# Optimization experiments

Hardware: AMD Instinct MI355X
Metric: run time of the kernel (lower is better)

Reference implementation:

```python
import jax, jax.numpy as jnp
import numpy as np

B, TX, TY, D, H, DK, DFF, L, V = 64, 200, 100, 512, 8, 64, 2048, 4, 30


def _ln(x, g, b, eps=1e-5):
    m = x.mean(-1, keepdims=True)
    v = x.var(-1, keepdims=True)  # biased, matches torch LayerNorm
    return (x - m) * jax.lax.rsqrt(v + eps) * g + b


def _mha(k_in, v_in, q_in, qkv, pw, pb, pad_mask, causal):
    # qkv: [3, H, DK, D] (torch Linear layout [out, in]); scale uses C = d_model
    scale = float(q_in.shape[-1]) ** 0.5
    Q = jnp.einsum('btd,hkd->bhtk', q_in, qkv[0])
    K = jnp.einsum('bsd,hkd->bhsk', k_in, qkv[1])
    Vv = jnp.einsum('bsd,hvd->bhsv', v_in, qkv[2])
    W = jnp.einsum('bhtk,bhsk->bhts', Q, K) / scale  # [B,H,T,S]
    if causal:
        tril = jnp.tril(jnp.ones((q_in.shape[1], k_in.shape[1]), bool))
        W = jnp.where(tril, W, -jnp.inf)
    if pad_mask is not None:
        W = jnp.where(pad_mask[:, None] == 1, -jnp.inf, W)
    A = jax.nn.softmax(W, axis=-1)
    out = jnp.einsum('bhts,bhsv->bhtv', A, Vv)
    b_, h_, t_, dv = out.shape
    out = out.transpose(0, 2, 1, 3).reshape(b_, t_, h_ * dv)  # concat heads
    return out @ pw.T + pb


def _attn_block(k, v, q, qkv, pw, pb, g, b, pad_mask, causal):
    kn, vn, qn = _ln(k, g, b), _ln(v, g, b), _ln(q, g, b)
    # NOTE: residual from the NORMED query, as in the original code
    return qn + _mha(kn, vn, qn, qkv, pw, pb, pad_mask, causal)


def _ff_block(x, w1, b1, w2, b2, g, b):
    h = jax.nn.relu(_ln(x, g, b) @ w1.T + b1)
    return x + h @ w2.T + b2


def _forward(x, y, enc_qkv, enc_proj_w, enc_proj_b, enc_ln1_g, enc_ln1_b,
             enc_ff_w1, enc_ff_b1, enc_ff_w2, enc_ff_b2, enc_ln2_g, enc_ln2_b,
             dec_sa_qkv, dec_sa_proj_w, dec_sa_proj_b, dec_ln1_g, dec_ln1_b,
             dec_ca_qkv, dec_ca_proj_w, dec_ca_proj_b, dec_ln2_g, dec_ln2_b,
             dec_ff_w1, dec_ff_b1, dec_ff_w2, dec_ff_b2, dec_ln3_g, dec_ln3_b,
             ll_w, ll_b, x_mask, y_mask):
    enc = x
    for i in range(L):
        enc = _attn_block(enc, enc, enc, enc_qkv[i], enc_proj_w[i], enc_proj_b[i],
                          enc_ln1_g[i], enc_ln1_b[i], x_mask, False)
        enc = _ff_block(enc, enc_ff_w1[i], enc_ff_b1[i], enc_ff_w2[i], enc_ff_b2[i],
                        enc_ln2_g[i], enc_ln2_b[i])
    dec = y
    for i in range(L):
        dec = _attn_block(dec, dec, dec, dec_sa_qkv[i], dec_sa_proj_w[i], dec_sa_proj_b[i],
                          dec_ln1_g[i], dec_ln1_b[i], y_mask, True)
        dec = _attn_block(enc, enc, dec, dec_ca_qkv[i], dec_ca_proj_w[i], dec_ca_proj_b[i],
                          dec_ln2_g[i], dec_ln2_b[i], None, False)
        dec = _ff_block(dec, dec_ff_w1[i], dec_ff_b1[i], dec_ff_w2[i], dec_ff_b2[i],
                        dec_ln3_g[i], dec_ln3_b[i])
    return dec @ ll_w.T + ll_b


def setup_inputs() -> dict:
    key = jax.random.key(0)
    ks = iter(jax.random.split(key, 64))

    def nrm(shape, s=0.02):
        return jax.random.normal(next(ks), shape, jnp.float32) * s

    return dict(
        x=nrm((B, TX, D), 1.0), y=nrm((B, TY, D), 1.0),
        x_mask=jnp.zeros((B, TX, TX), jnp.int32),
        y_mask=jnp.zeros((B, TY, TY), jnp.int32),
        enc_qkv=nrm((L, 3, H, DK, D)), enc_proj_w=nrm((L, D, D)), enc_proj_b=jnp.zeros((L, D)),
        enc_ln1_g=jnp.ones((L, D)), enc_ln1_b=jnp.zeros((L, D)),
        enc_ff_w1=nrm((L, DFF, D)), enc_ff_b1=jnp.zeros((L, DFF)),
        enc_ff_w2=nrm((L, D, DFF)), enc_ff_b2=jnp.zeros((L, D)),
        enc_ln2_g=jnp.ones((L, D)), enc_ln2_b=jnp.zeros((L, D)),
        dec_sa_qkv=nrm((L, 3, H, DK, D)), dec_sa_proj_w=nrm((L, D, D)), dec_sa_proj_b=jnp.zeros((L, D)),
        dec_ln1_g=jnp.ones((L, D)), dec_ln1_b=jnp.zeros((L, D)),
        dec_ca_qkv=nrm((L, 3, H, DK, D)), dec_ca_proj_w=nrm((L, D, D)), dec_ca_proj_b=jnp.zeros((L, D)),
        dec_ln2_g=jnp.ones((L, D)), dec_ln2_b=jnp.zeros((L, D)),
        dec_ff_w1=nrm((L, DFF, D)), dec_ff_b1=jnp.zeros((L, DFF)),
        dec_ff_w2=nrm((L, D, DFF)), dec_ff_b2=jnp.zeros((L, D)),
        dec_ln3_g=jnp.ones((L, D)), dec_ln3_b=jnp.zeros((L, D)),
        ll_w=nrm((V, D)), ll_b=jnp.zeros((V,)),
    )


def reference(x, y, x_mask, y_mask, enc_qkv, enc_proj_w, enc_proj_b, enc_ln1_g, enc_ln1_b,
              enc_ff_w1, enc_ff_b1, enc_ff_w2, enc_ff_b2, enc_ln2_g, enc_ln2_b,
              dec_sa_qkv, dec_sa_proj_w, dec_sa_proj_b, dec_ln1_g, dec_ln1_b,
              dec_ca_qkv, dec_ca_proj_w, dec_ca_proj_b, dec_ln2_g, dec_ln2_b,
              dec_ff_w1, dec_ff_b1, dec_ff_w2, dec_ff_b2, dec_ln3_g, dec_ln3_b,
              ll_w, ll_b):
    return _forward(x, y, enc_qkv, enc_proj_w, enc_proj_b, enc_ln1_g, enc_ln1_b,
                    enc_ff_w1, enc_ff_b1, enc_ff_w2, enc_ff_b2, enc_ln2_g, enc_ln2_b,
                    dec_sa_qkv, dec_sa_proj_w, dec_sa_proj_b, dec_ln1_g, dec_ln1_b,
                    dec_ca_qkv, dec_ca_proj_w, dec_ca_proj_b, dec_ln2_g, dec_ln2_b,
                    dec_ff_w1, dec_ff_b1, dec_ff_w2, dec_ff_b2, dec_ln3_g, dec_ln3_b,
                    ll_w, ll_b, x_mask, y_mask)
```

## Files before the change

### kernel.cpp

```cpp
#include <hip/hip_runtime.h>
#include <math.h>

#define B_SZ   64
#define TX_SZ  200
#define TY_SZ  100
#define D_MODEL 512
#define H_SZ   8
#define DK_SZ  64
#define DFF_SZ 2048
#define L_SZ   4
#define V_SZ   30

#define NEG_BIG -1.0e30f

#define KSTR  68
#define VSTR  212
#define PSTR  204
#define KOFF  0
#define VOFF  (200 * KSTR)
#define POFF  (VOFF + 64 * VSTR)
#define SMEMU (POFF + 4 * 16 * PSTR)

typedef unsigned short u16;
typedef __attribute__((ext_vector_type(8))) short short8;
typedef __attribute__((ext_vector_type(4))) short short4t;
typedef __attribute__((ext_vector_type(4))) float f32x4;
typedef __attribute__((ext_vector_type(4))) unsigned short u16x4;

__device__ __forceinline__ float b2f(u16 h) {
    union { unsigned int u; float f; } v; v.u = ((unsigned int)h) << 16; return v.f;
}
__device__ __forceinline__ u16 f2b(float f) {
    union { float f; unsigned int u; } v; v.f = f;
    unsigned int r = v.u + 0x7fffu + ((v.u >> 16) & 1u);
    return (u16)(r >> 16);
}
__device__ __forceinline__ short8 ld8(const u16* p) {
    short4t a = *(const short4t*)p;
    short4t b = *(const short4t*)(p + 4);
    return __builtin_shufflevector(a, b, 0, 1, 2, 3, 4, 5, 6, 7);
}

#define GLD16(gp, lp) __builtin_amdgcn_global_load_lds( \
    (const __attribute__((address_space(1))) unsigned int*)(gp), \
    (__attribute__((address_space(3))) unsigned int*)(lp), 16, 0, 0)

__global__ __launch_bounds__(256)
void castw_kernel(const float* __restrict__ in, u16* __restrict__ out, int n4) {
    int i = blockIdx.x * 256 + threadIdx.x;
    if (i < n4) {
        f32x4 v = ((const f32x4*)in)[i];
        u16x4 o;
        o.x = f2b(v.x); o.y = f2b(v.y); o.z = f2b(v.z); o.w = f2b(v.w);
        ((u16x4*)out)[i] = o;
    }
}

__global__ __launch_bounds__(256)
void ln_kernel(const float* __restrict__ in, const float* __restrict__ g,
               const float* __restrict__ b, float* outf, u16* outb, int rows) {
    int row = blockIdx.x * 4 + (threadIdx.x >> 6);
    int lane = threadIdx.x & 63;
    if (row >= rows) return;
    const f32x4* xr = (const f32x4*)(in + (size_t)row * D_MODEL);
    f32x4 v0 = xr[lane];
    f32x4 v1 = xr[lane + 64];
    float s  = v0.x + v0.y + v0.z + v0.w + v1.x + v1.y + v1.z + v1.w;
    float ss = v0.x*v0.x + v0.y*v0.y + v0.z*v0.z + v0.w*v0.w
             + v1.x*v1.x + v1.y*v1.y + v1.z*v1.z + v1.w*v1.w;
    #pragma unroll
    for (int off = 1; off < 64; off <<= 1) {
        s  += __shfl_xor(s, off, 64);
        ss += __shfl_xor(ss, off, 64);
    }
    float mean = s * (1.0f / D_MODEL);
    float var  = ss * (1.0f / D_MODEL) - mean * mean;
    float rstd = rsqrtf(var + 1e-5f);
    f32x4 g0 = ((const f32x4*)g)[lane],      g1 = ((const f32x4*)g)[lane + 64];
    f32x4 b0 = ((const f32x4*)b)[lane],      b1 = ((const f32x4*)b)[lane + 64];
    f32x4 o0, o1;
    o0.x = (v0.x - mean) * rstd * g0.x + b0.x;
    o0.y = (v0.y - mean) * rstd * g0.y + b0.y;
    o0.z = (v0.z - mean) * rstd * g0.z + b0.z;
    o0.w = (v0.w - mean) * rstd * g0.w + b0.w;
    o1.x = (v1.x - mean) * rstd * g1.x + b1.x;
    o1.y = (v1.y - mean) * rstd * g1.y + b1.y;
    o1.z = (v1.z - mean) * rstd * g1.z + b1.z;
    o1.w = (v1.w - mean) * rstd * g1.w + b1.w;
    if (outf) {
        f32x4* of = (f32x4*)(outf + (size_t)row * D_MODEL);
        of[lane] = o0; of[lane + 64] = o1;
    }
    if (outb) {
        u16x4* ob = (u16x4*)(outb + (size_t)row * D_MODEL);
        u16x4 p0, p1;
        p0.x = f2b(o0.x); p0.y = f2b(o0.y); p0.z = f2b(o0.z); p0.w = f2b(o0.w);
        p1.x = f2b(o1.x); p1.y = f2b(o1.y); p1.z = f2b(o1.z); p1.w = f2b(o1.w);
        ob[lane] = p0; ob[lane + 64] = p1;
    }
}

template<int BN>
__global__ __launch_bounds__(256)
void gemm_mfma_t(const u16* __restrict__ A, int lda,
                 const u16* __restrict__ W, int ldw,
                 float* outf, int ldcf, u16* outb, int ldcb,
                 const float* __restrict__ bias,
                 const float* __restrict__ resid, int ldr,
                 int relu, int K) {
    constexpr int NJ = BN / 32;
    __shared__ u16 Alds[128 * 32];
    __shared__ u16 Blds[BN * 32];
    const int tid  = threadIdx.x;
    const int wave = tid >> 6, lane = tid & 63;
    const int lr = lane & 15, lq = lane >> 4;
    const int wm = (wave >> 1) * 64, wn = (wave & 1) * (BN / 2);
    const int m0 = blockIdx.y * 128, n0 = blockIdx.x * BN;
    const int grow = tid >> 2;
    const int gcol = (tid & 3) * 8;
    const int woff = wave * 512;

    f32x4 zero = {0.f, 0.f, 0.f, 0.f};
    f32x4 acc[4][NJ];
    #pragma unroll
    for (int i = 0; i < 4; ++i)
        #pragma unroll
        for (int j = 0; j < NJ; ++j) acc[i][j] = zero;

    const u16* Ag = A + (size_t)m0 * lda;
    const u16* Wg = W + (size_t)n0 * ldw;

    for (int k0 = 0; k0 < K; k0 += 32) {
        GLD16(Ag + (size_t)grow * lda + k0 + gcol,        &Alds[woff]);
        GLD16(Ag + (size_t)(64 + grow) * lda + k0 + gcol, &Alds[2048 + woff]);
        GLD16(Wg + (size_t)grow * ldw + k0 + gcol,        &Blds[woff]);
        if (BN == 128)
            GLD16(Wg + (size_t)(64 + grow) * ldw + k0 + gcol, &Blds[2048 + woff]);
        __syncthreads();
        short8 af[4], bfr[NJ];
        #pragma unroll
        for (int i = 0; i < 4; ++i)
            af[i] = *(const short8*)&Alds[(wm + i * 16 + lr) * 32 + lq * 8];
        #pragma unroll
        for (int j = 0; j < NJ; ++j)
            bfr[j] = *(const short8*)&Blds[(wn + j * 16 + lr) * 32 + lq * 8];
        #pragma unroll
        for (int i = 0; i < 4; ++i)
            #pragma unroll
            for (int j = 0; j < NJ; ++j)
                acc[i][j] = __builtin_amdgcn_mfma_f32_16x16x32_bf16(af[i], bfr[j], acc[i][j], 0, 0, 0);
        __syncthreads();
    }

    #pragma unroll
    for (int i = 0; i < 4; ++i) {
        #pragma unroll
        for (int r = 0; r < 4; ++r) {
            int m = m0 + wm + i * 16 + lq * 4 + r;
            #pragma unroll
            for (int j = 0; j < NJ; ++j) {
                int n = n0 + wn + j * 16 + lr;
                float c = acc[i][j][r];
                if (bias)  c += bias[n];
                if (resid) c += resid[(size_t)m * ldr + n];
                if (relu)  c = fmaxf(c, 0.f);
                if (outf) outf[(size_t)m * ldcf + n] = c;
                if (outb) outb[(size_t)m * ldcb + n] = f2b(c);
            }
        }
    }
}

__global__ __launch_bounds__(256)
void attn_kernel(u16* __restrict__ Q, int ldq, const u16* __restrict__ K, int ldk,
                 const u16* __restrict__ V, int ldv,
                 const int* __restrict__ mask, int T, int S, int causal, float rscale) {
    __shared__ u16 smem[SMEMU];
    u16* Kl = smem + KOFF;
    u16* Vt = smem + VOFF;
    u16* Pl = smem + POFF;

    const int bh = blockIdx.x;
    const int h = bh % H_SZ, b = bh / H_SZ;
    const int tid = threadIdx.x, wave = tid >> 6, lane = tid & 63;
    const int lm = lane & 15, quad = lane >> 4;

    const u16* Kg = K + (size_t)(b * S) * ldk + h * DK_SZ;
    const u16* Vg = V + (size_t)(b * S) * ldv + h * DK_SZ;
    u16* Qg = Q + (size_t)(b * T) * ldq + h * DK_SZ;

    const int stiles = (S + 15) >> 4;
    const int Scols = stiles << 4;
    const int Pcap = (Scols < PSTR) ? Scols : PSTR;

    for (int i4 = tid * 4; i4 < S * DK_SZ; i4 += 1024) {
        int s = i4 >> 6, d = i4 & 63;
        u16x4 kv = *(const u16x4*)(Kg + (size_t)s * ldk + d);
        *(u16x4*)(Kl + s * KSTR + d) = kv;
        u16x4 vv = *(const u16x4*)(Vg + (size_t)s * ldv + d);
        Vt[(d + 0) * VSTR + s] = vv.x;
        Vt[(d + 1) * VSTR + s] = vv.y;
        Vt[(d + 2) * VSTR + s] = vv.z;
        Vt[(d + 3) * VSTR + s] = vv.w;
    }
    int pad = Scols - S;
    for (int i = tid; i < pad * DK_SZ; i += 256) {
        int d = i / pad, s = S + (i % pad);
        Vt[d * VSTR + s] = 0;
    }
    __syncthreads();

    const short8 zero8 = {0, 0, 0, 0, 0, 0, 0, 0};
    const f32x4 zerof = {0.f, 0.f, 0.f, 0.f};
    u16* Pw = Pl + wave * (16 * PSTR);

    for (int t0 = wave * 16; t0 < T; t0 += 64) {
        int qr = t0 + lm; if (qr >= T) qr = T - 1;
        const u16* qrow = Qg + (size_t)qr * ldq;
        short8 qa0 = *(const short8*)(qrow + quad * 8);
        short8 qa1 = *(const short8*)(qrow + 32 + quad * 8);

        f32x4 sc[13];
        #pragma unroll
        for (int st = 0; st < 13; ++st) if (st < stiles) {
            int srow = st * 16 + lm; if (srow >= S) srow = S - 1;
            const u16* kp = Kl + srow * KSTR + quad * 8;
            short8 kb0 = ld8(kp);
            short8 kb1 = ld8(kp + 32);
            f32x4 c = zerof;
            c = __builtin_amdgcn_mfma_f32_16x16x32_bf16(qa0, kb0, c, 0, 0, 0);
            c = __builtin_amdgcn_mfma_f32_16x16x32_bf16(qa1, kb1, c, 0, 0, 0);
            sc[st] = c;
        }

        float mx[4] = {NEG_BIG, NEG_BIG, NEG_BIG, NEG_BIG};
        #pragma unroll
        for (int st = 0; st < 13; ++st) if (st < stiles) {
            int s = st * 16 + lm;
            int smi = (s < S) ? s : S - 1;
            #pragma unroll
            for (int r = 0; r < 4; ++r) {
                int t = t0 + quad * 4 + r;
                int tc = (t < T) ? t : T - 1;
                bool valid = (s < S) && (!causal || s <= t);
                if (valid && mask) valid = (mask[(size_t)(b * T + tc) * S + smi] != 1);
                float f = valid ? sc[st][r] * rscale : NEG_BIG;
                sc[st][r] = f;
                mx[r] = fmaxf(mx[r], f);
            }
        }
        #pragma unroll
        for (int r = 0; r < 4; ++r) {
            #pragma unroll
            for (int off = 1; off < 16; off <<= 1)
                mx[r] = fmaxf(mx[r], __shfl_xor(mx[r], off, 64));
        }

        float sum[4] = {0.f, 0.f, 0.f, 0.f};
        #pragma unroll
        for (int st = 0; st < 13; ++st) if (st < stiles) {
            int col = st * 16 + lm;
            #pragma unroll
            for (int r = 0; r < 4; ++r) {
                float p = __expf(sc[st][r] - mx[r]);
                sum[r] += p;
                if (col < PSTR) Pw[(quad * 4 + r) * PSTR + col] = f2b(p);
            }
        }
        float rden[4];
        #pragma unroll
        for (int r = 0; r < 4; ++r) {
            #pragma unroll
            for (int off = 1; off < 16; off <<= 1)
                sum[r] += __shfl_xor(sum[r], off, 64);
            rden[r] = (sum[r] > 0.f) ? 1.0f / sum[r] : 0.f;
        }

        f32x4 ov[4] = {zerof, zerof, zerof, zerof};
        for (int k0 = 0; k0 < Pcap; k0 += 32) {
            int nq = (Pcap - k0) >> 3;
            short8 pa = (quad < nq) ? ld8(Pw + lm * PSTR + k0 + quad * 8) : zero8;
            #pragma unroll
            for (int dt = 0; dt < 4; ++dt) {
                short8 vb = (quad < nq)
                    ? ld8(Vt + (dt * 16 + lm) * VSTR + k0 + quad * 8)
                    : zero8;
                ov[dt] = __builtin_amdgcn_mfma_f32_16x16x32_bf16(pa, vb, ov[dt], 0, 0, 0);
            }
        }

        #pragma unroll
        for (int r = 0; r < 4; ++r) {
            int t = t0 + quad * 4 + r;
            if (t < T) {
                u16* orow = Qg + (size_t)t * ldq;
                #pragma unroll
                for (int dt = 0; dt < 4; ++dt)
                    orow[dt * 16 + lm] = f2b(ov[dt][r] * rden[r]);
            }
        }
    }
}

__global__ __launch_bounds__(256)
void logits_kernel(const float* __restrict__ X, const float* __restrict__ Wl,
                   const float* __restrict__ bl, float* __restrict__ out, int rows) {
    int idx = blockIdx.x * 256 + threadIdx.x;
    if (idx >= rows * V_SZ) return;
    int row = idx / V_SZ, v = idx % V_SZ;
    const f32x4* xr = (const f32x4*)(X + (size_t)row * D_MODEL);
    const f32x4* wr = (const f32x4*)(Wl + (size_t)v * D_MODEL);
    float acc = bl[v];
    #pragma unroll 4
    for (int k = 0; k < D_MODEL / 4; ++k) {
        f32x4 a = xr[k], w = wr[k];
        acc += a.x * w.x + a.y * w.y + a.z * w.z + a.w * w.w;
    }
    out[idx] = acc;
}

extern "C" void kernel_launch(void* const* d_in, const int* in_sizes, int n_in,
                              void* d_out, int out_size, void* d_ws, size_t ws_size,
                              hipStream_t stream) {
    const float* x          = (const float*)d_in[0];
    const float* y          = (const float*)d_in[1];
    const int*   x_mask     = (const int*)d_in[2];
    const int*   y_mask     = (const int*)d_in[3];
    const float* enc_qkv    = (const float*)d_in[4];
    const float* enc_proj_w = (const float*)d_in[5];
    const float* enc_proj_b = (const float*)d_in[6];
    const float* enc_ln1_g  = (const float*)d_in[7];
    const float* enc_ln1_b  = (const float*)d_in[8];
    const float* enc_ff_w1  = (const float*)d_in[9];
    const float* enc_ff_b1  = (const float*)d_in[10];
    const float* enc_ff_w2  = (const float*)d_in[11];
    const float* enc_ff_b2  = (const float*)d_in[12];
    const float* enc_ln2_g  = (const float*)d_in[13];
    const float* enc_ln2_b  = (const float*)d_in[14];
    const float* dec_sa_qkv    = (const float*)d_in[15];
    const float* dec_sa_proj_w = (const float*)d_in[16];
    const float* dec_sa_proj_b = (const float*)d_in[17];
    const float* dec_ln1_g  = (const float*)d_in[18];
    const float* dec_ln1_b  = (const float*)d_in[19];
    const float* dec_ca_qkv    = (const float*)d_in[20];
    const float* dec_ca_proj_w = (const float*)d_in[21];
    const float* dec_ca_proj_b = (const float*)d_in[22];
    const float* dec_ln2_g  = (const float*)d_in[23];
    const float* dec_ln2_b  = (const float*)d_in[24];
    const float* dec_ff_w1  = (const float*)d_in[25];
    const float* dec_ff_b1  = (const float*)d_in[26];
    const float* dec_ff_w2  = (const float*)d_in[27];
    const float* dec_ff_b2  = (const float*)d_in[28];
    const float* dec_ln3_g  = (const float*)d_in[29];
    const float* dec_ln3_b  = (const float*)d_in[30];
    const float* ll_w       = (const float*)d_in[31];
    const float* ll_b       = (const float*)d_in[32];

    const int ME = B_SZ * TX_SZ;
    const int MD = B_SZ * TY_SZ;
    const float rscale = 1.0f / sqrtf((float)D_MODEL);

    char* base = (char*)d_ws;
    size_t off = 0;
    auto alloc = [&](size_t bytes) {
        void* p = base + off;
        off = (off + bytes + 63) & ~(size_t)63;
        return p;
    };
    float* A_enc = (float*)alloc((size_t)ME * D_MODEL * 4);
    float* A_dec = (float*)alloc((size_t)MD * D_MODEL * 4);
    float* N1f   = (float*)alloc((size_t)ME * D_MODEL * 4);
    u16*   N1b   = (u16*)  alloc((size_t)ME * D_MODEL * 2);
    u16*   NQb   = (u16*)  alloc((size_t)MD * D_MODEL * 2);
    u16*   BIG   = (u16*)  alloc((size_t)ME * DFF_SZ * 2);
    u16*   Wa    = (u16*)  alloc((size_t)DFF_SZ * D_MODEL * 2);
    u16*   Wb2   = (u16*)  alloc((size_t)DFF_SZ * D_MODEL * 2);
    u16* QKVb = BIG;
    u16* Hb   = BIG;
    u16* KVb  = BIG;
    u16* Qca  = BIG + (size_t)ME * 1024;

    auto castw = [&](const float* in, u16* out, int n) {
        int n4 = n / 4;
        hipLaunchKernelGGL(castw_kernel, dim3((n4 + 255) / 256), dim3(256), 0, stream, in, out, n4);
    };
    auto ln = [&](const float* in, const float* g, const float* b,
                  float* outf, u16* outb, int rows) {
        hipLaunchKernelGGL(ln_kernel, dim3(rows / 4), dim3(256), 0, stream, in, g, b, outf, outb, rows);
    };
    auto gemm = [&](const u16* A, int lda, const u16* W, int ldw, int M, int N, int K,
                    float* outf, int ldcf, u16* outb, int ldcb,
                    const float* bias, const float* resid, int ldr, int relu) {
        int blocks128 = (M / 128) * (N / 128);
        if (blocks128 < 256) {
            dim3 grid(N / 64, M / 128);
            hipLaunchKernelGGL((gemm_mfma_t<64>), grid, dim3(256), 0, stream,
                               A, lda, W, ldw, outf, ldcf, outb, ldcb, bias, resid, ldr, relu, K);
        } else {
            dim3 grid(N / 128, M / 128);
            hipLaunchKernelGGL((gemm_mfma_t<128>), grid, dim3(256), 0, stream,
                               A, lda, W, ldw, outf, ldcf, outb, ldcb, bias, resid, ldr, relu, K);
        }
    };
    auto attn = [&](u16* Q, int ldq, const u16* K, int ldk, const u16* V, int ldv,
                    const int* mask, int T, int S, int causal) {
        hipLaunchKernelGGL(attn_kernel, dim3(B_SZ * H_SZ), dim3(256), 0, stream,
                           Q, ldq, K, ldk, V, ldv, mask, T, S, causal, rscale);
    };

    const int WQKV = 3 * D_MODEL * D_MODEL;
    const int WDD  = D_MODEL * D_MODEL;
    const int WFF  = DFF_SZ * D_MODEL;

    for (int l = 0; l < L_SZ; ++l) {
        const float* src = (l == 0) ? x : A_enc;
        castw(enc_qkv + (size_t)l * WQKV, Wa, WQKV);
        ln(src, enc_ln1_g + l * D_MODEL, enc_ln1_b + l * D_MODEL, N1f, N1b, ME);
        gemm(N1b, 512, Wa, 512, ME, 1536, 512, nullptr, 0, QKVb, 1536, nullptr, nullptr, 0, 0);
        attn(QKVb, 1536, QKVb + 512, 1536, QKVb + 1024, 1536, x_mask, TX_SZ, TX_SZ, 0);
        castw(enc_proj_w + (size_t)l * WDD, Wa, WDD);
        gemm(QKVb, 1536, Wa, 512, ME, 512, 512, A_enc, 512, nullptr, 0,
             enc_proj_b + l * D_MODEL, N1f, 512, 0);
        ln(A_enc, enc_ln2_g + l * D_MODEL, enc_ln2_b + l * D_MODEL, nullptr, N1b, ME);
        castw(enc_ff_w1 + (size_t)l * WFF, Wa, WFF);
        gemm(N1b, 512, Wa, 512, ME, 2048, 512, nullptr, 0, Hb, 2048,
             enc_ff_b1 + l * DFF_SZ, nullptr, 0, 1);
        castw(enc_ff_w2 + (size_t)l * WFF, Wb2, WFF);
        gemm(Hb, 2048, Wb2, 2048, ME, 512, 2048, A_enc, 512, nullptr, 0,
             enc_ff_b2 + l * D_MODEL, A_enc, 512, 0);
    }

    for (int l = 0; l < L_SZ; ++l) {
        const float* src = (l == 0) ? y : A_dec;
        castw(dec_sa_qkv + (size_t)l * WQKV, Wa, WQKV);
        ln(src, dec_ln1_g + l * D_MODEL, dec_ln1_b + l * D_MODEL, N1f, N1b, MD);
        gemm(N1b, 512, Wa, 512, MD, 1536, 512, nullptr, 0, QKVb, 1536, nullptr, nullptr, 0, 0);
        attn(QKVb, 1536, QKVb + 512, 1536, QKVb + 1024, 1536, y_mask, TY_SZ, TY_SZ, 1);
        castw(dec_sa_proj_w + (size_t)l * WDD, Wa, WDD);
        gemm(QKVb, 1536, Wa, 512, MD, 512, 512, A_dec, 512, nullptr, 0,
             dec_sa_proj_b + l * D_MODEL, N1f, 512, 0);
        ln(A_enc, dec_ln2_g + l * D_MODEL, dec_ln2_b + l * D_MODEL, nullptr, N1b, ME);
        ln(A_dec, dec_ln2_g + l * D_MODEL, dec_ln2_b + l * D_MODEL, N1f, NQb, MD);
        castw(dec_ca_qkv + (size_t)l * WQKV, Wa, WDD);
        gemm(NQb, 512, Wa, 512, MD, 512, 512, nullptr, 0, Qca, 512, nullptr, nullptr, 0, 0);
        castw(dec_ca_qkv + (size_t)l * WQKV + WDD, Wa, 2 * WDD);
        gemm(N1b, 512, Wa, 512, ME, 1024, 512, nullptr, 0, KVb, 1024, nullptr, nullptr, 0, 0);
        attn(Qca, 512, KVb, 1024, KVb + 512, 1024, nullptr, TY_SZ, TX_SZ, 0);
        castw(dec_ca_proj_w + (size_t)l * WDD, Wa, WDD);
        gemm(Qca, 512, Wa, 512, MD, 512, 512, A_dec, 512, nullptr, 0,
             dec_ca_proj_b + l * D_MODEL, N1f, 512, 0);
        ln(A_dec, dec_ln3_g + l * D_MODEL, dec_ln3_b + l * D_MODEL, nullptr, N1b, MD);
        castw(dec_ff_w1 + (size_t)l * WFF, Wa, WFF);
        gemm(N1b, 512, Wa, 512, MD, 2048, 512, nullptr, 0, Hb, 2048,
             dec_ff_b1 + l * DFF_SZ, nullptr, 0, 1);
        castw(dec_ff_w2 + (size_t)l * WFF, Wb2, WFF);
        gemm(Hb, 2048, Wb2, 2048, MD, 512, 2048, A_dec, 512, nullptr, 0,
             dec_ff_b2 + l * D_MODEL, A_dec, 512, 0);
    }

    {
        int total = MD * V_SZ;
        hipLaunchKernelGGL(logits_kernel, dim3((total + 255) / 256), dim3(256), 0, stream,
                           A_dec, ll_w, ll_b, (float*)d_out, MD);
    }
    (void)in_sizes; (void)n_in; (void)out_size; (void)ws_size;
}
```

Baseline: 3.197 ms.

## Write V transposed from QKV GEMM epilogue and split attention over query tiles

The QKV and KV GEMM epilogues now scatter the V columns directly into a per-(batch,head) transposed buffer, so attention no longer stages and transposes K/V in LDS. The attention grid is split into 64-row query tiles per (batch,head), with K and Vt read straight from global memory, and causal tiles skip key tiles past the diagonal. This removes the per-block LDS transpose and raises parallelism. The cost is scattered strided stores in the GEMM epilogue, uncached global K/V reads repeated across tiles, and an extra pad kernel for the decoder case.

New measurement: 3.468 ms. 8.5% more time.

```diff
diff --git a/kernel.cpp b/kernel.cpp
--- a/kernel.cpp
+++ b/kernel.cpp
@@ -13,13 +13,8 @@
 
 #define NEG_BIG -1.0e30f
 
-#define KSTR  68
-#define VSTR  212
 #define PSTR  204
-#define KOFF  0
-#define VOFF  (200 * KSTR)
-#define POFF  (VOFF + 64 * VSTR)
-#define SMEMU (POFF + 4 * 16 * PSTR)
+#define ATT_LDSU (4 * 16 * PSTR)
 
 typedef unsigned short u16;
 typedef __attribute__((ext_vector_type(8))) short short8;
@@ -53,6 +48,16 @@
         u16x4 o;
         o.x = f2b(v.x); o.y = f2b(v.y); o.z = f2b(v.z); o.w = f2b(v.w);
         ((u16x4*)out)[i] = o;
+    }
+}
+
+__global__ __launch_bounds__(256)
+void vtpad_kernel(u16* __restrict__ Vt, int spad, int S, int nrows) {
+    int pad = spad - S;
+    int i = blockIdx.x * 256 + threadIdx.x;
+    if (i < nrows * pad) {
+        int r = i / pad, c = i - r * pad;
+        Vt[(size_t)r * spad + S + c] = 0;
     }
 }
 
@@ -107,7 +112,9 @@
                  float* outf, int ldcf, u16* outb, int ldcb,
                  const float* __restrict__ bias,
                  const float* __restrict__ resid, int ldr,
-                 int relu, int K) {
+                 int relu, int K,
+                 u16* __restrict__ vtout, int vt_n0, int vt_T,
+                 unsigned rT, int vt_spad) {
     constexpr int NJ = BN / 32;
     __shared__ u16 Alds[128 * 32];
     __shared__ u16 Blds[BN * 32];
@@ -165,7 +172,14 @@
                 if (resid) c += resid[(size_t)m * ldr + n];
                 if (relu)  c = fmaxf(c, 0.f);
                 if (outf) outf[(size_t)m * ldcf + n] = c;
-                if (outb) outb[(size_t)m * ldcb + n] = f2b(c);
+                if (vtout && n >= vt_n0) {
+                    int hd = n - vt_n0;
+                    int bq = (int)(((unsigned)m * rT) >> 22);
+                    int sq = m - bq * vt_T;
+                    vtout[((size_t)((bq << 3) + (hd >> 6)) * 64 + (hd & 63)) * vt_spad + sq] = f2b(c);
+                } else if (outb) {
+                    outb[(size_t)m * ldcb + n] = f2b(c);
+                }
             }
         }
     }
@@ -173,131 +187,113 @@
 
 __global__ __launch_bounds__(256)
 void attn_kernel(u16* __restrict__ Q, int ldq, const u16* __restrict__ K, int ldk,
-                 const u16* __restrict__ V, int ldv,
+                 const u16* __restrict__ Vt, int spad,
                  const int* __restrict__ mask, int T, int S, int causal, float rscale) {
-    __shared__ u16 smem[SMEMU];
-    u16* Kl = smem + KOFF;
-    u16* Vt = smem + VOFF;
-    u16* Pl = smem + POFF;
-
-    const int bh = blockIdx.x;
-    const int h = bh % H_SZ, b = bh / H_SZ;
+    __shared__ u16 Pl[ATT_LDSU];
+    const int tile = blockIdx.x, bh = blockIdx.y;
+    const int h = bh & 7, b = bh >> 3;
     const int tid = threadIdx.x, wave = tid >> 6, lane = tid & 63;
     const int lm = lane & 15, quad = lane >> 4;
+    const int t0 = tile * 64 + wave * 16;
+    if (t0 >= T) return;
 
     const u16* Kg = K + (size_t)(b * S) * ldk + h * DK_SZ;
-    const u16* Vg = V + (size_t)(b * S) * ldv + h * DK_SZ;
+    const u16* Vg = Vt + (size_t)bh * 64 * spad;
     u16* Qg = Q + (size_t)(b * T) * ldq + h * DK_SZ;
 
     const int stiles = (S + 15) >> 4;
-    const int Scols = stiles << 4;
-    const int Pcap = (Scols < PSTR) ? Scols : PSTR;
-
-    for (int i4 = tid * 4; i4 < S * DK_SZ; i4 += 1024) {
-        int s = i4 >> 6, d = i4 & 63;
-        u16x4 kv = *(const u16x4*)(Kg + (size_t)s * ldk + d);
-        *(u16x4*)(Kl + s * KSTR + d) = kv;
-        u16x4 vv = *(const u16x4*)(Vg + (size_t)s * ldv + d);
-        Vt[(d + 0) * VSTR + s] = vv.x;
-        Vt[(d + 1) * VSTR + s] = vv.y;
-        Vt[(d + 2) * VSTR + s] = vv.z;
-        Vt[(d + 3) * VSTR + s] = vv.w;
-    }
-    int pad = Scols - S;
-    for (int i = tid; i < pad * DK_SZ; i += 256) {
-        int d = i / pad, s = S + (i % pad);
-        Vt[d * VSTR + s] = 0;
-    }
-    __syncthreads();
+    int stmax = stiles;
+    if (causal) { int c = (t0 >> 4) + 1; if (c < stmax) stmax = c; }
+    const int Scap8 = (S + 7) & ~7;
+    int Pcap = stmax * 16; if (Pcap > Scap8) Pcap = Scap8;
+
+    u16* Pw = Pl + wave * (16 * PSTR);
+
+    int qr = t0 + lm; if (qr >= T) qr = T - 1;
+    const u16* qrow = Qg + (size_t)qr * ldq;
+    short8 qa0 = *(const short8*)(qrow + quad * 8);
+    short8 qa1 = *(const short8*)(qrow + 32 + quad * 8);
 
     const short8 zero8 = {0, 0, 0, 0, 0, 0, 0, 0};
     const f32x4 zerof = {0.f, 0.f, 0.f, 0.f};
-    u16* Pw = Pl + wave * (16 * PSTR);
-
-    for (int t0 = wave * 16; t0 < T; t0 += 64) {
-        int qr = t0 + lm; if (qr >= T) qr = T - 1;
-        const u16* qrow = Qg + (size_t)qr * ldq;
-        short8 qa0 = *(const short8*)(qrow + quad * 8);
-        short8 qa1 = *(const short8*)(qrow + 32 + quad * 8);
-
-        f32x4 sc[13];
-        #pragma unroll
-        for (int st = 0; st < 13; ++st) if (st < stiles) {
-            int srow = st * 16 + lm; if (srow >= S) srow = S - 1;
-            const u16* kp = Kl + srow * KSTR + quad * 8;
-            short8 kb0 = ld8(kp);
-            short8 kb1 = ld8(kp + 32);
-            f32x4 c = zerof;
-            c = __builtin_amdgcn_mfma_f32_16x16x32_bf16(qa0, kb0, c, 0, 0, 0);
-            c = __builtin_amdgcn_mfma_f32_16x16x32_bf16(qa1, kb1, c, 0, 0, 0);
-            sc[st] = c;
-        }
-
-        float mx[4] = {NEG_BIG, NEG_BIG, NEG_BIG, NEG_BIG};
-        #pragma unroll
-        for (int st = 0; st < 13; ++st) if (st < stiles) {
-            int s = st * 16 + lm;
-            int smi = (s < S) ? s : S - 1;
-            #pragma unroll
-            for (int r = 0; r < 4; ++r) {
-                int t = t0 + quad * 4 + r;
-                int tc = (t < T) ? t : T - 1;
-                bool valid = (s < S) && (!causal || s <= t);
-                if (valid && mask) valid = (mask[(size_t)(b * T + tc) * S + smi] != 1);
-                float f = valid ? sc[st][r] * rscale : NEG_BIG;
-                sc[st][r] = f;
-                mx[r] = fmaxf(mx[r], f);
-            }
-        }
-        #pragma unroll
-        for (int r = 0; r < 4; ++r) {
-            #pragma unroll
-            for (int off = 1; off < 16; off <<= 1)
-                mx[r] = fmaxf(mx[r], __shfl_xor(mx[r], off, 64));
-        }
-
-        float sum[4] = {0.f, 0.f, 0.f, 0.f};
-        #pragma unroll
-        for (int st = 0; st < 13; ++st) if (st < stiles) {
-            int col = st * 16 + lm;
-            #pragma unroll
-            for (int r = 0; r < 4; ++r) {
-                float p = __expf(sc[st][r] - mx[r]);
-                sum[r] += p;
-                if (col < PSTR) Pw[(quad * 4 + r) * PSTR + col] = f2b(p);
-            }
-        }
-        float rden[4];
-        #pragma unroll
-        for (int r = 0; r < 4; ++r) {
-            #pragma unroll
-            for (int off = 1; off < 16; off <<= 1)
-                sum[r] += __shfl_xor(sum[r], off, 64);
-            rden[r] = (sum[r] > 0.f) ? 1.0f / sum[r] : 0.f;
-        }
-
-        f32x4 ov[4] = {zerof, zerof, zerof, zerof};
-        for (int k0 = 0; k0 < Pcap; k0 += 32) {
-            int nq = (Pcap - k0) >> 3;
-            short8 pa = (quad < nq) ? ld8(Pw + lm * PSTR + k0 + quad * 8) : zero8;
-            #pragma unroll
-            for (int dt = 0; dt < 4; ++dt) {
-                short8 vb = (quad < nq)
-                    ? ld8(Vt + (dt * 16 + lm) * VSTR + k0 + quad * 8)
-                    : zero8;
-                ov[dt] = __builtin_amdgcn_mfma_f32_16x16x32_bf16(pa, vb, ov[dt], 0, 0, 0);
-            }
-        }
-
+
+    f32x4 sc[13];
+    #pragma unroll
+    for (int st = 0; st < 13; ++st) if (st < stmax) {
+        int srow = st * 16 + lm; if (srow >= S) srow = S - 1;
+        const u16* kp = Kg + (size_t)srow * ldk + quad * 8;
+        short8 kb0 = *(const short8*)kp;
+        short8 kb1 = *(const short8*)(kp + 32);
+        f32x4 c = zerof;
+        c = __builtin_amdgcn_mfma_f32_16x16x32_bf16(qa0, kb0, c, 0, 0, 0);
+        c = __builtin_amdgcn_mfma_f32_16x16x32_bf16(qa1, kb1, c, 0, 0, 0);
+        sc[st] = c;
+    }
+
+    float mx[4] = {NEG_BIG, NEG_BIG, NEG_BIG, NEG_BIG};
+    #pragma unroll
+    for (int st = 0; st < 13; ++st) if (st < stmax) {
+        int s = st * 16 + lm;
+        int smi = (s < S) ? s : S - 1;
         #pragma unroll
         for (int r = 0; r < 4; ++r) {
             int t = t0 + quad * 4 + r;
-            if (t < T) {
-                u16* orow = Qg + (size_t)t * ldq;
-                #pragma unroll
-                for (int dt = 0; dt < 4; ++dt)
-                    orow[dt * 16 + lm] = f2b(ov[dt][r] * rden[r]);
-            }
+            int tc = (t < T) ? t : T - 1;
+            bool valid = (s < S) && (!causal || s <= t);
+            if (valid && mask) valid = (mask[(size_t)(b * T + tc) * S + smi] != 1);
+            float f = valid ? sc[st][r] * rscale : NEG_BIG;
+            sc[st][r] = f;
+            mx[r] = fmaxf(mx[r], f);
+        }
+    }
+    #pragma unroll
+    for (int r = 0; r < 4; ++r) {
+        #pragma unroll
+        for (int off = 1; off < 16; off <<= 1)
+            mx[r] = fmaxf(mx[r], __shfl_xor(mx[r], off, 64));
+    }
+
+    float sum[4] = {0.f, 0.f, 0.f, 0.f};
+    #pragma unroll
+    for (int st = 0; st < 13; ++st) if (st < stmax) {
+        int col = st * 16 + lm;
+        #pragma unroll
+        for (int r = 0; r < 4; ++r) {
+            float p = __expf(sc[st][r] - mx[r]);
+            sum[r] += p;
+            if (col < PSTR) Pw[(quad * 4 + r) * PSTR + col] = f2b(p);
+        }
+    }
+    float rden[4];
+    #pragma unroll
+    for (int r = 0; r < 4; ++r) {
+        #pragma unroll
+        for (int off = 1; off < 16; off <<= 1)
+            sum[r] += __shfl_xor(sum[r], off, 64);
+        rden[r] = (sum[r] > 0.f) ? 1.0f / sum[r] : 0.f;
+    }
+
+    f32x4 ov[4] = {zerof, zerof, zerof, zerof};
+    for (int k0 = 0; k0 < Pcap; k0 += 32) {
+        int nq = (Pcap - k0) >> 3;
+        short8 pa = (quad < nq) ? ld8(Pw + lm * PSTR + k0 + quad * 8) : zero8;
+        #pragma unroll
+        for (int dt = 0; dt < 4; ++dt) {
+            short8 vb = (quad < nq)
+                ? *(const short8*)(Vg + (size_t)(dt * 16 + lm) * spad + k0 + quad * 8)
+                : zero8;
+            ov[dt] = __builtin_amdgcn_mfma_f32_16x16x32_bf16(pa, vb, ov[dt], 0, 0, 0);
+        }
+    }
+
+    #pragma unroll
+    for (int r = 0; r < 4; ++r) {
+        int t = t0 + quad * 4 + r;
+        if (t < T) {
+            u16* orow = Qg + (size_t)t * ldq;
+            #pragma unroll
+            for (int dt = 0; dt < 4; ++dt)
+                orow[dt * 16 + lm] = f2b(ov[dt][r] * rden[r]);
         }
     }
 }
@@ -359,6 +355,8 @@
     const int ME = B_SZ * TX_SZ;
     const int MD = B_SZ * TY_SZ;
     const float rscale = 1.0f / sqrtf((float)D_MODEL);
+    const unsigned rT200 = (1u << 22) / 200 + 1;
+    const unsigned rT100 = (1u << 22) / 100 + 1;
 
     char* base = (char*)d_ws;
     size_t off = 0;
@@ -375,6 +373,7 @@
     u16*   BIG   = (u16*)  alloc((size_t)ME * DFF_SZ * 2);
     u16*   Wa    = (u16*)  alloc((size_t)DFF_SZ * D_MODEL * 2);
     u16*   Wb2   = (u16*)  alloc((size_t)DFF_SZ * D_MODEL * 2);
+    u16*   Vt    = (u16*)  alloc((size_t)B_SZ * H_SZ * 64 * 208 * 2);
     u16* QKVb = BIG;
     u16* Hb   = BIG;
     u16* KVb  = BIG;
@@ -388,24 +387,41 @@
                   float* outf, u16* outb, int rows) {
         hipLaunchKernelGGL(ln_kernel, dim3(rows / 4), dim3(256), 0, stream, in, g, b, outf, outb, rows);
     };
-    auto gemm = [&](const u16* A, int lda, const u16* W, int ldw, int M, int N, int K,
-                    float* outf, int ldcf, u16* outb, int ldcb,
-                    const float* bias, const float* resid, int ldr, int relu) {
+    auto gemm_full = [&](const u16* A, int lda, const u16* W, int ldw, int M, int N, int K,
+                         float* outf, int ldcf, u16* outb, int ldcb,
+                         const float* bias, const float* resid, int ldr, int relu,
+                         u16* vtout, int vt_n0, int vt_T, unsigned rT, int vt_spad) {
         int blocks128 = (M / 128) * (N / 128);
         if (blocks128 < 256) {
             dim3 grid(N / 64, M / 128);
             hipLaunchKernelGGL((gemm_mfma_t<64>), grid, dim3(256), 0, stream,
-                               A, lda, W, ldw, outf, ldcf, outb, ldcb, bias, resid, ldr, relu, K);
+                               A, lda, W, ldw, outf, ldcf, outb, ldcb, bias, resid, ldr, relu, K,
+                               vtout, vt_n0, vt_T, rT, vt_spad);
         } else {
             dim3 grid(N / 128, M / 128);
             hipLaunchKernelGGL((gemm_mfma_t<128>), grid, dim3(256), 0, stream,
-                               A, lda, W, ldw, outf, ldcf, outb, ldcb, bias, resid, ldr, relu, K);
-        }
-    };
-    auto attn = [&](u16* Q, int ldq, const u16* K, int ldk, const u16* V, int ldv,
+                               A, lda, W, ldw, outf, ldcf, outb, ldcb, bias, resid, ldr, relu, K,
+                               vtout, vt_n0, vt_T, rT, vt_spad);
+        }
+    };
+    auto gemm = [&](const u16* A, int lda, const u16* W, int ldw, int M, int N, int K,
+                    float* outf, int ldcf, u16* outb, int ldcb,
+                    const float* bias, const float* resid, int ldr, int relu) {
+        gemm_full(A, lda, W, ldw, M, N, K, outf, ldcf, outb, ldcb, bias, resid, ldr, relu,
+                  nullptr, 0, 1, 0, 1);
+    };
+    auto vtpad = [&](u16* vt, int spad, int S) {
+        int pad = spad - S;
+        if (pad <= 0) return;
+        int tot = B_SZ * H_SZ * 64 * pad;
+        hipLaunchKernelGGL(vtpad_kernel, dim3((tot + 255) / 256), dim3(256), 0, stream,
+                           vt, spad, S, B_SZ * H_SZ * 64);
+    };
+    auto attn = [&](u16* Q, int ldq, const u16* K, int ldk, const u16* vt, int spad,
                     const int* mask, int T, int S, int causal) {
-        hipLaunchKernelGGL(attn_kernel, dim3(B_SZ * H_SZ), dim3(256), 0, stream,
-                           Q, ldq, K, ldk, V, ldv, mask, T, S, causal, rscale);
+        dim3 grid((T + 63) / 64, B_SZ * H_SZ);
+        hipLaunchKernelGGL(attn_kernel, grid, dim3(256), 0, stream,
+                           Q, ldq, K, ldk, vt, spad, mask, T, S, causal, rscale);
     };
 
     const int WQKV = 3 * D_MODEL * D_MODEL;
@@ -416,8 +432,9 @@
         const float* src = (l == 0) ? x : A_enc;
         castw(enc_qkv + (size_t)l * WQKV, Wa, WQKV);
         ln(src, enc_ln1_g + l * D_MODEL, enc_ln1_b + l * D_MODEL, N1f, N1b, ME);
-        gemm(N1b, 512, Wa, 512, ME, 1536, 512, nullptr, 0, QKVb, 1536, nullptr, nullptr, 0, 0);
-        attn(QKVb, 1536, QKVb + 512, 1536, QKVb + 1024, 1536, x_mask, TX_SZ, TX_SZ, 0);
+        gemm_full(N1b, 512, Wa, 512, ME, 1536, 512, nullptr, 0, QKVb, 1536,
+                  nullptr, nullptr, 0, 0, Vt, 1024, TX_SZ, rT200, 200);
+        attn(QKVb, 1536, QKVb + 512, 1536, Vt, 200, x_mask, TX_SZ, TX_SZ, 0);
         castw(enc_proj_w + (size_t)l * WDD, Wa, WDD);
         gemm(QKVb, 1536, Wa, 512, ME, 512, 512, A_enc, 512, nullptr, 0,
              enc_proj_b + l * D_MODEL, N1f, 512, 0);
@@ -434,8 +451,10 @@
         const float* src = (l == 0) ? y : A_dec;
         castw(dec_sa_qkv + (size_t)l * WQKV, Wa, WQKV);
         ln(src, dec_ln1_g + l * D_MODEL, dec_ln1_b + l * D_MODEL, N1f, N1b, MD);
-        gemm(N1b, 512, Wa, 512, MD, 1536, 512, nullptr, 0, QKVb, 1536, nullptr, nullptr, 0, 0);
-        attn(QKVb, 1536, QKVb + 512, 1536, QKVb + 1024, 1536, y_mask, TY_SZ, TY_SZ, 1);
+        gemm_full(N1b, 512, Wa, 512, MD, 1536, 512, nullptr, 0, QKVb, 1536,
+                  nullptr, nullptr, 0, 0, Vt, 1024, TY_SZ, rT100, 104);
+        vtpad(Vt, 104, 100);
+        attn(QKVb, 1536, QKVb + 512, 1536, Vt, 104, y_mask, TY_SZ, TY_SZ, 1);
         castw(dec_sa_proj_w + (size_t)l * WDD, Wa, WDD);
         gemm(QKVb, 1536, Wa, 512, MD, 512, 512, A_dec, 512, nullptr, 0,
              dec_sa_proj_b + l * D_MODEL, N1f, 512, 0);
@@ -444,8 +463,9 @@
         castw(dec_ca_qkv + (size_t)l * WQKV, Wa, WDD);
         gemm(NQb, 512, Wa, 512, MD, 512, 512, nullptr, 0, Qca, 512, nullptr, nullptr, 0, 0);
         castw(dec_ca_qkv + (size_t)l * WQKV + WDD, Wa, 2 * WDD);
-        gemm(N1b, 512, Wa, 512, ME, 1024, 512, nullptr, 0, KVb, 1024, nullptr, nullptr, 0, 0);
-        attn(Qca, 512, KVb, 1024, KVb + 512, 1024, nullptr, TY_SZ, TX_SZ, 0);
+        gemm_full(N1b, 512, Wa, 512, ME, 1024, 512, nullptr, 0, KVb, 1024,
+                  nullptr, nullptr, 0, 0, Vt, 512, TX_SZ, rT200, 200);
+        attn(Qca, 512, KVb, 1024, Vt, 200, nullptr, TY_SZ, TX_SZ, 0);
         castw(dec_ca_proj_w + (size_t)l * WDD, Wa, WDD);
         gemm(Qca, 512, Wa, 512, MD, 512, 512, A_dec, 512, nullptr, 0,
              dec_ca_proj_b + l * D_MODEL, N1f, 512, 0);
```
